# Optimization experiments

Measured on AMD Instinct MI355X. Metric: run time of the kernel, lower is better.

## Reference

```python
import jax, jax.numpy as jnp
import numpy as np
from jax import lax

B = 32        # true batch size (groups)
C_IN = 64     # per-sample input channels
C_OUT = 64    # per-sample output channels
H = W = 256
KH = KW = 3


def setup_inputs() -> dict:
    key = jax.random.key(0)
    kx, kk = jax.random.split(key)
    # x folds the batch into channels: [1, B*C_in, H, W]
    x = jax.random.normal(kx, (1, B * C_IN, H, W), dtype=jnp.float32)
    # per-sample kernels stacked along output-filter axis: [B*C_out, C_in, kH, kW]
    kernels = jax.random.normal(kk, (B * C_OUT, C_IN, KH, KW), dtype=jnp.float32)
    return {"x": x, "kernels": kernels, "batch_size": B}


def reference(x, kernels, batch_size):
    # F.conv2d(x, kernels, stride=1, padding='same', groups=batch_size)
    # Grouped conv with feature_group_count = batch_size (one group per sample).
    out = lax.conv_general_dilated(
        x,
        kernels,
        window_strides=(1, 1),
        padding="SAME",
        feature_group_count=batch_size,
        dimension_numbers=("NCHW", "OIHW", "NCHW"),
    )
    return out
```

## Files before the change

### kernel.cpp

```cpp
#include <hip/hip_runtime.h>
#include <hip/hip_bf16.h>


typedef __bf16 bf16x8 __attribute__((ext_vector_type(8)));
typedef float  f32x4  __attribute__((ext_vector_type(4)));

#define NB 32
#define NH 256
#define NW 256
#define TILE_H 8
#define TILE_W 64
#define XROWS 10
#define XCOLS 68
#define HWSZ ((size_t)NH * NW)

__global__ void repack_weights_kernel(const float* __restrict__ wsrc,
                                      __bf16* __restrict__ pk) {
    int t = blockIdx.x * blockDim.x + threadIdx.x;
    if (t >= NB * 9 * 4 * 2 * 64) return;
    int lane = t & 63;
    int r = t >> 6;
    int kc = r & 1;  r >>= 1;
    int mt = r & 3;  r >>= 2;
    int tap = r % 9;
    int b   = r / 9;
    int co  = b * 64 + mt * 16 + (lane & 15);
    int ci0 = kc * 32 + (lane >> 4) * 8;
    bf16x8 v;
#pragma unroll
    for (int j = 0; j < 8; ++j) {
        v[j] = (__bf16)wsrc[(co * 64 + ci0 + j) * 9 + tap];
    }
    *reinterpret_cast<bf16x8*>(pk + (size_t)t * 8) = v;
}

__launch_bounds__(512)
__global__ void conv_mfma_kernel(const float* __restrict__ x,
                                 const __bf16* __restrict__ pk,
                                 float* __restrict__ out) {
    __shared__ __align__(16) __bf16 xs[XROWS * XCOLS * 32];

    const int orig = blockIdx.x;
    const int wg   = (orig & 7) * 512 + (orig >> 3);
    const int b    = wg >> 7;
    const int by   = (wg >> 2) & 31;
    const int bx   = wg & 3;
    const int h0   = by * TILE_H;
    const int w0   = bx * TILE_W;

    const int tid  = threadIdx.x;
    const int wid  = tid >> 6;
    const int lane = tid & 63;
    const int nl   = lane & 15;
    const int kgrp = lane >> 4;

    const __bf16* pkb = pk + (size_t)b * 9 * 4096;

    bf16x8 af[4][4];
    auto load_af = [&](int g) {
        const int tap = (g >= 9) ? g - 9 : g;
        const int kc  = (g >= 9) ? 1 : 0;
        const int sl  = g & 3;
#pragma unroll
        for (int mt = 0; mt < 4; ++mt)
            af[sl][mt] = *reinterpret_cast<const bf16x8*>(
                pkb + tap * 4096 + ((mt * 2 + kc) * 64 + lane) * 8);
    };

    load_af(0);
    load_af(1);

    f32x4 acc[4][4];
#pragma unroll
    for (int mt = 0; mt < 4; ++mt)
#pragma unroll
        for (int q = 0; q < 4; ++q)
            acc[mt][q] = (f32x4){0.f, 0.f, 0.f, 0.f};

    const int c     = lane;
    const int w     = w0 - 1 + c;
    const int wcl   = min(max(w, 0), NW - 1);
    const bool wbad = (w != wcl);
    const int oct   = wid & 3;
    const int rbase = (wid >> 2) * 5;
    const int sciw  = ((oct ^ ((c >> 1) & 3)) * 8);

    const int hr    = tid >> 3;
    const int hside = (tid >> 2) & 1;
    const int hoct  = tid & 3;
    const int hch   = 64 + hside;
    const int hw    = w0 + 63 + hside;
    const int hwc   = min(hw, NW - 1);

#pragma unroll
    for (int kc = 0; kc < 2; ++kc) {
        {
            const int cibase = b * 64 + kc * 32 + oct * 8;
            const float* colp = x + (size_t)cibase * HWSZ + wcl;

            float hv[8];
            if (tid < 80) {
                const int h  = h0 - 1 + hr;
                const int hc = min(max(h, 0), NH - 1);
                const float* src = x + ((size_t)(b * 64 + kc * 32 + hoct * 8) * NH + hc) * NW + hwc;
#pragma unroll
                for (int j = 0; j < 8; ++j) hv[j] = src[j * HWSZ];
                if (h != hc || hw != hwc) {
#pragma unroll
                    for (int j = 0; j < 8; ++j) hv[j] = 0.f;
                }
            }

            float va[8], vb[8], vc[8];
            auto load8 = [&](int r, float* v) {
                const int h  = h0 - 1 + rbase + r;
                const int hc = min(max(h, 0), NH - 1);
                const float* src = colp + (size_t)hc * NW;
#pragma unroll
                for (int j = 0; j < 8; ++j) v[j] = src[j * HWSZ];
                if (wbad || h != hc) {
#pragma unroll
                    for (int j = 0; j < 8; ++j) v[j] = 0.f;
                }
            };
            auto store8 = [&](int r, const float* v) {
                const int rr = rbase + r;
                bf16x8 o;
#pragma unroll
                for (int j = 0; j < 8; ++j) o[j] = (__bf16)v[j];
                *reinterpret_cast<bf16x8*>(xs + (rr * XCOLS + c) * 32 + sciw) = o;
            };

            load8(0, va);
            load8(1, vb);
            load8(2, vc);
            store8(0, va); load8(3, va);
            store8(1, vb); load8(4, vb);
            store8(2, vc);
            store8(3, va);
            store8(4, vb);

            if (tid < 80) {
                bf16x8 o;
#pragma unroll
                for (int j = 0; j < 8; ++j) o[j] = (__bf16)hv[j];
                *reinterpret_cast<bf16x8*>(xs + (hr * XCOLS + hch) * 32 + hoct * 8) = o;
            }
        }
        __syncthreads();

#pragma unroll
        for (int tap = 0; tap < 9; ++tap) {
            const int g = kc * 9 + tap;
            if (g + 2 < 18) load_af(g + 2);
            const int kh = tap / 3;
            const int kw = tap - kh * 3;
            const int rowbase = (wid + kh) * XCOLS;
            const int fs = g & 3;
#pragma unroll
            for (int q = 0; q < 4; ++q) {
                const int cc   = q * 16 + nl + kw;
                const int slot = (cc >> 1) & 3;
                bf16x8 bfv = *reinterpret_cast<const bf16x8*>(
                    xs + (rowbase + cc) * 32 + ((kgrp ^ slot) * 8));
#pragma unroll
                for (int mt = 0; mt < 4; ++mt)
                    acc[mt][q] = __builtin_amdgcn_mfma_f32_16x16x32_bf16(
                        af[fs][mt], bfv, acc[mt][q], 0, 0, 0);
            }
        }
        if (kc == 0) __syncthreads();
    }

    const int mrow = kgrp * 4;
    const int h = h0 + wid;
#pragma unroll
    for (int mt = 0; mt < 4; ++mt) {
#pragma unroll
        for (int q = 0; q < 4; ++q) {
            const int ww = w0 + q * 16 + nl;
#pragma unroll
            for (int rg = 0; rg < 4; ++rg) {
                const int co = mt * 16 + mrow + rg;
                out[((size_t)(b * 64 + co) * NH + h) * NW + ww] = acc[mt][q][rg];
            }
        }
    }
}

extern "C" void kernel_launch(void* const* d_in, const int* in_sizes, int n_in,
                              void* d_out, int out_size, void* d_ws, size_t ws_size,
                              hipStream_t stream) {
    const float* x = (const float*)d_in[0];
    const float* w = (const float*)d_in[1];
    float* out = (float*)d_out;
    __bf16* pk = (__bf16*)d_ws;

    {
        int total = NB * 9 * 4 * 2 * 64;
        int blk = 256;
        int grid = (total + blk - 1) / blk;
        hipLaunchKernelGGL(repack_weights_kernel, dim3(grid), dim3(blk), 0, stream,
                           w, pk);
    }
    {
        dim3 grid(4096);
        hipLaunchKernelGGL(conv_mfma_kernel, grid, dim3(512), 0, stream,
                           x, pk, out);
    }
}
```

Baseline: 319.2 us.

## Stage per-chunk weight fragments in LDS and alternate channel-chunk order per block

Weight fragments for each 32-channel chunk are now copied cooperatively into shared memory alongside the input tile, and each wave reads its A fragments from LDS instead of holding a rolling register prefetch from global memory. Odd and even workgroups process the two channel chunks in opposite order, spreading global reads across different addresses. The LDS input row pitch shrinks from 68 to 66 columns and launch bounds request 4 blocks per SM. The intent is to cut redundant global weight loads and register pressure. In exchange it adds about 36KB of LDS per block, which may limit occupancy, plus extra LDS traffic and a barrier.

```diff
diff --git a/kernel.cpp b/kernel.cpp
--- a/kernel.cpp
+++ b/kernel.cpp
@@ -11,7 +11,7 @@
 #define TILE_H 8
 #define TILE_W 64
 #define XROWS 10
-#define XCOLS 68
+#define XCOLS 66
 #define HWSZ ((size_t)NH * NW)
 
 __global__ void repack_weights_kernel(const float* __restrict__ wsrc,
@@ -34,11 +34,12 @@
     *reinterpret_cast<bf16x8*>(pk + (size_t)t * 8) = v;
 }
 
-__launch_bounds__(512)
+__launch_bounds__(512, 4)
 __global__ void conv_mfma_kernel(const float* __restrict__ x,
                                  const __bf16* __restrict__ pk,
                                  float* __restrict__ out) {
     __shared__ __align__(16) __bf16 xs[XROWS * XCOLS * 32];
+    __shared__ __align__(16) __bf16 afs[36 * 512];
 
     const int orig = blockIdx.x;
     const int wg   = (orig & 7) * 512 + (orig >> 3);
@@ -54,21 +55,7 @@
     const int nl   = lane & 15;
     const int kgrp = lane >> 4;
 
-    const __bf16* pkb = pk + (size_t)b * 9 * 4096;
-
-    bf16x8 af[4][4];
-    auto load_af = [&](int g) {
-        const int tap = (g >= 9) ? g - 9 : g;
-        const int kc  = (g >= 9) ? 1 : 0;
-        const int sl  = g & 3;
-#pragma unroll
-        for (int mt = 0; mt < 4; ++mt)
-            af[sl][mt] = *reinterpret_cast<const bf16x8*>(
-                pkb + tap * 4096 + ((mt * 2 + kc) * 64 + lane) * 8);
-    };
-
-    load_af(0);
-    load_af(1);
+    const __bf16* pkb = pk + (size_t)b * 36864;
 
     f32x4 acc[4][4];
 #pragma unroll
@@ -92,71 +79,83 @@
     const int hw    = w0 + 63 + hside;
     const int hwc   = min(hw, NW - 1);
 
-#pragma unroll
-    for (int kc = 0; kc < 2; ++kc) {
-        {
-            const int cibase = b * 64 + kc * 32 + oct * 8;
-            const float* colp = x + (size_t)cibase * HWSZ + wcl;
-
-            float hv[8];
-            if (tid < 80) {
-                const int h  = h0 - 1 + hr;
-                const int hc = min(max(h, 0), NH - 1);
-                const float* src = x + ((size_t)(b * 64 + kc * 32 + hoct * 8) * NH + hc) * NW + hwc;
-#pragma unroll
-                for (int j = 0; j < 8; ++j) hv[j] = src[j * HWSZ];
-                if (h != hc || hw != hwc) {
-#pragma unroll
-                    for (int j = 0; j < 8; ++j) hv[j] = 0.f;
-                }
-            }
-
-            float va[8], vb[8], vc[8];
-            auto load8 = [&](int r, float* v) {
-                const int h  = h0 - 1 + rbase + r;
-                const int hc = min(max(h, 0), NH - 1);
-                const float* src = colp + (size_t)hc * NW;
-#pragma unroll
-                for (int j = 0; j < 8; ++j) v[j] = src[j * HWSZ];
-                if (wbad || h != hc) {
-#pragma unroll
-                    for (int j = 0; j < 8; ++j) v[j] = 0.f;
-                }
-            };
-            auto store8 = [&](int r, const float* v) {
-                const int rr = rbase + r;
-                bf16x8 o;
-#pragma unroll
-                for (int j = 0; j < 8; ++j) o[j] = (__bf16)v[j];
-                *reinterpret_cast<bf16x8*>(xs + (rr * XCOLS + c) * 32 + sciw) = o;
-            };
-
-            load8(0, va);
-            load8(1, vb);
-            load8(2, vc);
-            store8(0, va); load8(3, va);
-            store8(1, vb); load8(4, vb);
-            store8(2, vc);
-            store8(3, va);
-            store8(4, vb);
-
-            if (tid < 80) {
-                bf16x8 o;
-#pragma unroll
-                for (int j = 0; j < 8; ++j) o[j] = (__bf16)hv[j];
-                *reinterpret_cast<bf16x8*>(xs + (hr * XCOLS + hch) * 32 + hoct * 8) = o;
-            }
-        }
-        __syncthreads();
-
+    auto stage = [&](int kcv) {
+#pragma unroll
+        for (int i = 0; i < 5; ++i) {
+            const int idx = tid + i * 512;
+            if (i < 4 || tid < 256) {
+                const int f = idx >> 6;
+                const int wo = idx & 63;
+                bf16x8 v = *reinterpret_cast<const bf16x8*>(
+                    pkb + ((size_t)(f * 2 + kcv) * 512 + wo * 8));
+                *reinterpret_cast<bf16x8*>(afs + f * 512 + wo * 8) = v;
+            }
+        }
+
+        const int cibase = b * 64 + kcv * 32 + oct * 8;
+        const float* colp = x + (size_t)cibase * HWSZ + wcl;
+
+        float hv[8];
+        if (tid < 80) {
+            const int h  = h0 - 1 + hr;
+            const int hc = min(max(h, 0), NH - 1);
+            const float* src = x + ((size_t)(b * 64 + kcv * 32 + hoct * 8) * NH + hc) * NW + hwc;
+#pragma unroll
+            for (int j = 0; j < 8; ++j) hv[j] = src[j * HWSZ];
+            if (h != hc || hw != hwc) {
+#pragma unroll
+                for (int j = 0; j < 8; ++j) hv[j] = 0.f;
+            }
+        }
+
+        float va[8], vb[8], vc[8];
+        auto load8 = [&](int r, float* v) {
+            const int h  = h0 - 1 + rbase + r;
+            const int hc = min(max(h, 0), NH - 1);
+            const float* src = colp + (size_t)hc * NW;
+#pragma unroll
+            for (int j = 0; j < 8; ++j) v[j] = src[j * HWSZ];
+            if (wbad || h != hc) {
+#pragma unroll
+                for (int j = 0; j < 8; ++j) v[j] = 0.f;
+            }
+        };
+        auto store8 = [&](int r, const float* v) {
+            const int rr = rbase + r;
+            bf16x8 o;
+#pragma unroll
+            for (int j = 0; j < 8; ++j) o[j] = (__bf16)v[j];
+            *reinterpret_cast<bf16x8*>(xs + (rr * XCOLS + c) * 32 + sciw) = o;
+        };
+
+        load8(0, va);
+        load8(1, vb);
+        load8(2, vc);
+        store8(0, va); load8(3, va);
+        store8(1, vb); load8(4, vb);
+        store8(2, vc);
+        store8(3, va);
+        store8(4, vb);
+
+        if (tid < 80) {
+            bf16x8 o;
+#pragma unroll
+            for (int j = 0; j < 8; ++j) o[j] = (__bf16)hv[j];
+            *reinterpret_cast<bf16x8*>(xs + (hr * XCOLS + hch) * 32 + hoct * 8) = o;
+        }
+    };
+
+    auto compute = [&]() {
 #pragma unroll
         for (int tap = 0; tap < 9; ++tap) {
-            const int g = kc * 9 + tap;
-            if (g + 2 < 18) load_af(g + 2);
+            bf16x8 afr[4];
+#pragma unroll
+            for (int mt = 0; mt < 4; ++mt)
+                afr[mt] = *reinterpret_cast<const bf16x8*>(
+                    afs + (tap * 4 + mt) * 512 + lane * 8);
             const int kh = tap / 3;
             const int kw = tap - kh * 3;
             const int rowbase = (wid + kh) * XCOLS;
-            const int fs = g & 3;
 #pragma unroll
             for (int q = 0; q < 4; ++q) {
                 const int cc   = q * 16 + nl + kw;
@@ -166,11 +165,19 @@
 #pragma unroll
                 for (int mt = 0; mt < 4; ++mt)
                     acc[mt][q] = __builtin_amdgcn_mfma_f32_16x16x32_bf16(
-                        af[fs][mt], bfv, acc[mt][q], 0, 0, 0);
-            }
-        }
-        if (kc == 0) __syncthreads();
-    }
+                        afr[mt], bfv, acc[mt][q], 0, 0, 0);
+            }
+        }
+    };
+
+    const int par = wg & 1;
+    stage(par);
+    __syncthreads();
+    compute();
+    __syncthreads();
+    stage(par ^ 1);
+    __syncthreads();
+    compute();
 
     const int mrow = kgrp * 4;
     const int h = h0 + wid;
```

Result: slower. 499.7 us (+56.6%).
